# Performance work log

Measured on AMD Instinct MI355X. Metric: run time of the kernel, lower is better.

Reference implementation:

```python
import jax, jax.numpy as jnp
import numpy as np


def setup_inputs() -> dict:
    key = jax.random.key(0)
    k1, k2, k3, k4 = jax.random.split(key, 4)
    B, T, C, H = 8, 2048, 1024, 64
    x = jax.random.normal(k1, (B, T, C), dtype=jnp.float32)
    # nn.Linear weights, stored as (in, out) for x @ W
    Wk = jax.random.normal(k2, (C, H), dtype=jnp.float32) * (C ** -0.5)
    Wq = jax.random.normal(k3, (C, H), dtype=jnp.float32) * (C ** -0.5)
    Wv = jax.random.normal(k4, (C, H), dtype=jnp.float32) * (C ** -0.5)
    return {"x": x, "Wk": Wk, "Wq": Wq, "Wv": Wv}


def reference(x, Wk, Wq, Wv):
    B, T, C = x.shape
    k = x @ Wk  # [B,T,H]
    q = x @ Wq  # [B,T,H]
    v = x @ Wv  # [B,T,H]
    # NOTE: original scales by C**-0.5 (full embed dim), not head_size**-0.5
    wei = jnp.einsum("bth,bsh->bts", q, k) * (C ** -0.5)  # [B,T,T]
    causal = jnp.tril(jnp.ones((T, T), dtype=bool))
    wei = jnp.where(causal, wei, -jnp.inf)
    wei = jax.nn.softmax(wei, axis=-1)
    # dropout is identity in eval/reference mode
    out = jnp.einsum("bts,bsh->bth", wei, v)  # [B,T,H]
    return out
```

## Files before the change

### kernel.cpp

```cpp
#include <hip/hip_runtime.h>
#include <hip/hip_bf16.h>
#include <math.h>

#define B_ 8
#define T_ 2048
#define C_ 1024
#define H_ 64
#define M_ (B_*T_)

typedef __attribute__((ext_vector_type(8))) short short8;
typedef __attribute__((ext_vector_type(4))) float f32x4;
typedef unsigned int u32;

__device__ __forceinline__ unsigned short f2bf(float f) {
    u32 u = __builtin_bit_cast(u32, f);
    u += 0x7FFFu + ((u >> 16) & 1u);
    return (unsigned short)(u >> 16);
}

__device__ __forceinline__ void gl2lds16(const void* g, void* l) {
    __builtin_amdgcn_global_load_lds(
        (const __attribute__((address_space(1))) u32*)g,
        (__attribute__((address_space(3))) u32*)l, 16, 0, 0);
}

__global__ __launch_bounds__(256) void wconv(
    const float* __restrict__ Wk, const float* __restrict__ Wq,
    const float* __restrict__ Wv, unsigned short* __restrict__ wb)
{
    __shared__ unsigned short lt[64][64];
    const int mat = blockIdx.x >> 4;
    const int k0  = (blockIdx.x & 15) * 64;
    const float* src = (mat == 0) ? Wk : (mat == 1 ? Wq : Wv);
    const float sc = (mat == 1) ? 0.03125f : 1.0f;
    const int tid = threadIdx.x;

    for (int it = 0; it < 16; ++it) {
        int idx = it * 256 + tid;
        int r = idx >> 6, cn = idx & 63;
        lt[cn][r] = f2bf(src[(size_t)(k0 + r) * H_ + cn] * sc);
    }
    __syncthreads();
    for (int g = 0; g < 2; ++g) {
        int n  = g * 32 + (tid >> 3);
        int kp = tid & 7;
        int ng = mat * 64 + n;
        short8 v = *reinterpret_cast<const short8*>(&lt[n][kp * 8]);
        char* dst = (char*)wb + (size_t)ng * 2048 + (k0 >> 6) * 128
                  + ((kp * 16) ^ ((ng & 7) << 4));
        *reinterpret_cast<short8*>(dst) = v;
    }
}

__global__ __launch_bounds__(256, 2) void qkv_mm(
    const float* __restrict__ x, const unsigned short* __restrict__ wb,
    unsigned short* __restrict__ kb, unsigned short* __restrict__ qb,
    unsigned short* __restrict__ vT)
{
    __shared__ __align__(16) unsigned short Ws[2][96 * 64];

    const int tid  = threadIdx.x;
    const int wid  = tid >> 6;
    const int lane = tid & 63;
    const int lr   = lane & 15;
    const int lg   = lane >> 4;
    const int mt   = blockIdx.x >> 1;
    const int bn   = blockIdx.x & 1;
    const int m0   = mt * 64;
    const int n0   = bn * 96;

    const float* xrow = x + (size_t)(m0 + wid * 16 + lr) * C_ + lg * 8;

    f32x4 acc[6];
    for (int c = 0; c < 6; ++c) acc[c] = (f32x4){0.f, 0.f, 0.f, 0.f};

    float4 xa = *reinterpret_cast<const float4*>(xrow);
    float4 xb2 = *reinterpret_cast<const float4*>(xrow + 4);
    float4 xc = *reinterpret_cast<const float4*>(xrow + 32);
    float4 xd = *reinterpret_cast<const float4*>(xrow + 36);
    for (int p = 0; p < 3; ++p) {
        int c = p * 256 + tid;
        gl2lds16((const char*)wb + (size_t)(n0 + (c >> 3)) * 2048 + (c & 7) * 16,
                 (char*)&Ws[0][0] + c * 16);
    }

    for (int t = 0; t < 16; ++t) {
        __syncthreads();
        float4 na, nb, nc, nd;
        if (t < 15) {
            const float* xn = xrow + (t + 1) * 64;
            na = *reinterpret_cast<const float4*>(xn);
            nb = *reinterpret_cast<const float4*>(xn + 4);
            nc = *reinterpret_cast<const float4*>(xn + 32);
            nd = *reinterpret_cast<const float4*>(xn + 36);
            int buf = (t + 1) & 1;
            for (int p = 0; p < 3; ++p) {
                int c = p * 256 + tid;
                gl2lds16((const char*)wb + (size_t)(n0 + (c >> 3)) * 2048
                             + (size_t)(t + 1) * 128 + (c & 7) * 16,
                         (char*)&Ws[buf][0] + c * 16);
            }
        }

        short8 af0, af1;
        af0[0] = (short)f2bf(xa.x); af0[1] = (short)f2bf(xa.y);
        af0[2] = (short)f2bf(xa.z); af0[3] = (short)f2bf(xa.w);
        af0[4] = (short)f2bf(xb2.x); af0[5] = (short)f2bf(xb2.y);
        af0[6] = (short)f2bf(xb2.z); af0[7] = (short)f2bf(xb2.w);
        af1[0] = (short)f2bf(xc.x); af1[1] = (short)f2bf(xc.y);
        af1[2] = (short)f2bf(xc.z); af1[3] = (short)f2bf(xc.w);
        af1[4] = (short)f2bf(xd.x); af1[5] = (short)f2bf(xd.y);
        af1[6] = (short)f2bf(xd.z); af1[7] = (short)f2bf(xd.w);

        const char* wbuf = (const char*)&Ws[t & 1][0];
        #pragma unroll
        for (int kc = 0; kc < 2; ++kc) {
            short8 afc = kc ? af1 : af0;
            #pragma unroll
            for (int ct = 0; ct < 6; ++ct) {
                int n = ct * 16 + lr;
                short8 bf = *reinterpret_cast<const short8*>(
                    wbuf + n * 128 + ((kc * 64 + lg * 16) ^ ((n & 7) << 4)));
                acc[ct] = __builtin_amdgcn_mfma_f32_16x16x32_bf16(afc, bf, acc[ct], 0, 0, 0);
            }
        }
        xa = na; xb2 = nb; xc = nc; xd = nd;
    }

    for (int ct = 0; ct < 6; ++ct) {
        int ng = n0 + ct * 16 + lr;
        int col = ng & 63;
        for (int i = 0; i < 4; ++i) {
            int m = m0 + wid * 16 + lg * 4 + i;
            unsigned short val = f2bf(acc[ct][i]);
            if (ng < 64)       kb[(size_t)m * H_ + col] = val;
            else if (ng < 128) qb[(size_t)m * H_ + col] = val;
            else               vT[((size_t)(m >> 11) * H_ + col) * T_ + (m & (T_ - 1))] = val;
        }
    }
}

__global__ __launch_bounds__(256, 2) void attn4(
    const unsigned short* __restrict__ kb,
    const unsigned short* __restrict__ qb,
    const unsigned short* __restrict__ vT,
    float* __restrict__ out)
{
    __shared__ __align__(16) unsigned short Ps[4][16][72];
    __shared__ float Om[4][16][64];
    __shared__ float Mv[4][16], Lv[4][16], Fac[4][16], InvL[16];

    const int tid  = threadIdx.x;
    const int wid  = tid >> 6;
    const int lane = tid & 63;
    const int lr   = lane & 15;
    const int lg   = lane >> 4;
    const int b    = blockIdx.y;
    const int bx   = blockIdx.x;
    const int tile = (bx & 1) ? (127 - (bx >> 1)) : (bx >> 1);
    const int q0   = tile * 16;
    const int nsteps = (tile >> 2) + 1;
    const size_t base = (size_t)b * T_ * H_;
    const unsigned short* vTb = vT + (size_t)b * H_ * T_;

    short8 qf[2];
    #pragma unroll
    for (int kc = 0; kc < 2; ++kc)
        qf[kc] = *reinterpret_cast<const short8*>(
            qb + base + (size_t)(q0 + lr) * H_ + kc * 32 + lg * 8);

    f32x4 o[4];
    float mrun[4], lrun[4];
    for (int dt = 0; dt < 4; ++dt) o[dt] = (f32x4){0.f, 0.f, 0.f, 0.f};
    for (int i = 0; i < 4; ++i) { mrun[i] = -INFINITY; lrun[i] = 0.f; }

    for (int s = wid; s < nsteps; s += 4) {
        const int kv0 = s * 64;

        short8 kf[2][4];
        #pragma unroll
        for (int kc = 0; kc < 2; ++kc)
            #pragma unroll
            for (int kt = 0; kt < 4; ++kt)
                kf[kc][kt] = *reinterpret_cast<const short8*>(
                    kb + base + (size_t)(kv0 + kt * 16 + lr) * H_ + kc * 32 + lg * 8);

        f32x4 sv4[4];
        for (int kt = 0; kt < 4; ++kt) sv4[kt] = (f32x4){0.f, 0.f, 0.f, 0.f};
        #pragma unroll
        for (int kc = 0; kc < 2; ++kc)
            #pragma unroll
            for (int kt = 0; kt < 4; ++kt)
                sv4[kt] = __builtin_amdgcn_mfma_f32_16x16x32_bf16(qf[kc], kf[kc][kt], sv4[kt], 0, 0, 0);

        short8 vf[2][4];
        #pragma unroll
        for (int kc = 0; kc < 2; ++kc)
            #pragma unroll
            for (int dt = 0; dt < 4; ++dt)
                vf[kc][dt] = *reinterpret_cast<const short8*>(
                    vTb + (size_t)(dt * 16 + lr) * T_ + kv0 + kc * 32 + lg * 8);

        const bool need_mask = (s == nsteps - 1);

        for (int i = 0; i < 4; ++i) {
            int row = q0 + lg * 4 + i;
            float sv[4];
            float mx = -INFINITY;
            if (need_mask) {
                for (int kt = 0; kt < 4; ++kt) {
                    int key = kv0 + kt * 16 + lr;
                    float v = (key <= row) ? sv4[kt][i] : -INFINITY;
                    sv[kt] = v;
                    mx = fmaxf(mx, v);
                }
            } else {
                for (int kt = 0; kt < 4; ++kt) {
                    sv[kt] = sv4[kt][i];
                    mx = fmaxf(mx, sv[kt]);
                }
            }
            for (int d = 8; d; d >>= 1) mx = fmaxf(mx, __shfl_xor(mx, d));
            float mn  = fmaxf(mrun[i], mx);
            float fac = __expf(mrun[i] - mn);
            float rs  = 0.f;
            for (int kt = 0; kt < 4; ++kt) {
                float p = __expf(sv[kt] - mn);
                rs += p;
                Ps[wid][lg * 4 + i][kt * 16 + lr] = f2bf(p);
            }
            for (int d = 8; d; d >>= 1) rs += __shfl_xor(rs, d);
            lrun[i] = lrun[i] * fac + rs;
            mrun[i] = mn;
            for (int dt = 0; dt < 4; ++dt)
                o[dt][i] *= fac;
        }

        #pragma unroll
        for (int kc = 0; kc < 2; ++kc) {
            short8 pf = *reinterpret_cast<const short8*>(&Ps[wid][lr][kc * 32 + lg * 8]);
            #pragma unroll
            for (int dt = 0; dt < 4; ++dt)
                o[dt] = __builtin_amdgcn_mfma_f32_16x16x32_bf16(pf, vf[kc][dt], o[dt], 0, 0, 0);
        }
    }

    for (int dt = 0; dt < 4; ++dt)
        for (int i = 0; i < 4; ++i)
            Om[wid][lg * 4 + i][dt * 16 + lr] = o[dt][i];
    if (lr == 0)
        for (int i = 0; i < 4; ++i) {
            Mv[wid][lg * 4 + i] = mrun[i];
            Lv[wid][lg * 4 + i] = lrun[i];
        }
    __syncthreads();
    if (tid < 16) {
        float M = Mv[0][tid];
        for (int w = 1; w < 4; ++w) M = fmaxf(M, Mv[w][tid]);
        float L = 0.f;
        for (int w = 0; w < 4; ++w) {
            float f = __expf(Mv[w][tid] - M);
            Fac[w][tid] = f;
            L += Lv[w][tid] * f;
        }
        InvL[tid] = 1.0f / L;
    }
    __syncthreads();
    for (int e = 0; e < 4; ++e) {
        int idx = e * 256 + tid;
        int row = idx >> 6, d = idx & 63;
        float v = 0.f;
        for (int w = 0; w < 4; ++w) v += Om[w][row][d] * Fac[w][row];
        out[base + (size_t)(q0 + row) * H_ + d] = v * InvL[row];
    }
}

extern "C" void kernel_launch(void* const* d_in, const int* in_sizes, int n_in,
                              void* d_out, int out_size, void* d_ws, size_t ws_size,
                              hipStream_t stream) {
    const float* x  = (const float*)d_in[0];
    const float* Wk = (const float*)d_in[1];
    const float* Wq = (const float*)d_in[2];
    const float* Wv = (const float*)d_in[3];
    float* out = (float*)d_out;

    unsigned short* kb = (unsigned short*)d_ws;
    unsigned short* qb = kb + (size_t)M_ * H_;
    unsigned short* vT = qb + (size_t)M_ * H_;
    unsigned short* wb = vT + (size_t)M_ * H_;

    wconv<<<48, 256, 0, stream>>>(Wk, Wq, Wv, wb);
    qkv_mm<<<512, 256, 0, stream>>>(x, wb, kb, qb, vT);
    attn4<<<dim3(128, B_), 256, 0, stream>>>(kb, qb, vT, out);
}
```

Measured before the change: 179.5 us.

## Widen QKV GEMM tile, pipeline loads, split attention into single-wave blocks plus merge

```diff
diff --git a/kernel.cpp b/kernel.cpp
--- a/kernel.cpp
+++ b/kernel.cpp
@@ -16,6 +16,10 @@
     u32 u = __builtin_bit_cast(u32, f);
     u += 0x7FFFu + ((u >> 16) & 1u);
     return (unsigned short)(u >> 16);
+}
+__device__ __forceinline__ float bf2f(unsigned short h) {
+    u32 u = ((u32)h) << 16;
+    return __builtin_bit_cast(float, u);
 }
 
 __device__ __forceinline__ void gl2lds16(const void* g, void* l) {
@@ -52,114 +56,119 @@
     }
 }
 
-__global__ __launch_bounds__(256, 2) void qkv_mm(
+#define LOADX(R0,R1,R2,R3,t) {                                        \
+    const float* p_ = xrow + (t) * 64;                                \
+    R0 = *reinterpret_cast<const float4*>(p_);                        \
+    R1 = *reinterpret_cast<const float4*>(p_ + 4);                    \
+    R2 = *reinterpret_cast<const float4*>(p_ + 32);                   \
+    R3 = *reinterpret_cast<const float4*>(p_ + 36); }
+
+#define STAGEW(buf, t) {                                              \
+    _Pragma("unroll") for (int p_ = 0; p_ < 6; ++p_) {                \
+        int c_ = p_ * 256 + tid;                                      \
+        gl2lds16((const char*)wb + (size_t)(c_ >> 3) * 2048           \
+                     + (size_t)(t) * 128 + (c_ & 7) * 16,             \
+                 (char*)&Ws[buf][0] + c_ * 16);                       \
+    } }
+
+__global__ __launch_bounds__(256) void qkv_mm(
     const float* __restrict__ x, const unsigned short* __restrict__ wb,
     unsigned short* __restrict__ kb, unsigned short* __restrict__ qb,
     unsigned short* __restrict__ vT)
 {
-    __shared__ __align__(16) unsigned short Ws[2][96 * 64];
+    __shared__ __align__(16) unsigned short Ws[2][192 * 64];
 
     const int tid  = threadIdx.x;
     const int wid  = tid >> 6;
     const int lane = tid & 63;
     const int lr   = lane & 15;
     const int lg   = lane >> 4;
-    const int mt   = blockIdx.x >> 1;
-    const int bn   = blockIdx.x & 1;
-    const int m0   = mt * 64;
-    const int n0   = bn * 96;
+    const int m0   = blockIdx.x * 64;
 
     const float* xrow = x + (size_t)(m0 + wid * 16 + lr) * C_ + lg * 8;
 
-    f32x4 acc[6];
-    for (int c = 0; c < 6; ++c) acc[c] = (f32x4){0.f, 0.f, 0.f, 0.f};
-
-    float4 xa = *reinterpret_cast<const float4*>(xrow);
-    float4 xb2 = *reinterpret_cast<const float4*>(xrow + 4);
-    float4 xc = *reinterpret_cast<const float4*>(xrow + 32);
-    float4 xd = *reinterpret_cast<const float4*>(xrow + 36);
-    for (int p = 0; p < 3; ++p) {
-        int c = p * 256 + tid;
-        gl2lds16((const char*)wb + (size_t)(n0 + (c >> 3)) * 2048 + (c & 7) * 16,
-                 (char*)&Ws[0][0] + c * 16);
-    }
-
+    f32x4 acc[12];
+    #pragma unroll
+    for (int c = 0; c < 12; ++c) acc[c] = (f32x4){0.f, 0.f, 0.f, 0.f};
+
+    float4 xA0, xA1, xA2, xA3, xB0, xB1, xB2, xB3, xC0, xC1, xC2, xC3;
+
+    LOADX(xA0, xA1, xA2, xA3, 0);
+    __builtin_amdgcn_sched_barrier(0);
+    STAGEW(0, 0);
+    __builtin_amdgcn_sched_barrier(0);
+    LOADX(xB0, xB1, xB2, xB3, 1);
+    __builtin_amdgcn_sched_barrier(0);
+
+    #pragma unroll
     for (int t = 0; t < 16; ++t) {
-        __syncthreads();
-        float4 na, nb, nc, nd;
-        if (t < 15) {
-            const float* xn = xrow + (t + 1) * 64;
-            na = *reinterpret_cast<const float4*>(xn);
-            nb = *reinterpret_cast<const float4*>(xn + 4);
-            nc = *reinterpret_cast<const float4*>(xn + 32);
-            nd = *reinterpret_cast<const float4*>(xn + 36);
-            int buf = (t + 1) & 1;
-            for (int p = 0; p < 3; ++p) {
-                int c = p * 256 + tid;
-                gl2lds16((const char*)wb + (size_t)(n0 + (c >> 3)) * 2048
-                             + (size_t)(t + 1) * 128 + (c & 7) * 16,
-                         (char*)&Ws[buf][0] + c * 16);
-            }
-        }
+        if (t < 15) asm volatile("s_waitcnt vmcnt(4) lgkmcnt(0)" ::: "memory");
+        else        asm volatile("s_waitcnt vmcnt(0) lgkmcnt(0)" ::: "memory");
+        __builtin_amdgcn_s_barrier();
+        __builtin_amdgcn_sched_barrier(0);
+        if (t < 15) { STAGEW((t + 1) & 1, t + 1); }
+        __builtin_amdgcn_sched_barrier(0);
+        if (t < 14) { LOADX(xC0, xC1, xC2, xC3, t + 2); }
+        __builtin_amdgcn_sched_barrier(0);
 
         short8 af0, af1;
-        af0[0] = (short)f2bf(xa.x); af0[1] = (short)f2bf(xa.y);
-        af0[2] = (short)f2bf(xa.z); af0[3] = (short)f2bf(xa.w);
-        af0[4] = (short)f2bf(xb2.x); af0[5] = (short)f2bf(xb2.y);
-        af0[6] = (short)f2bf(xb2.z); af0[7] = (short)f2bf(xb2.w);
-        af1[0] = (short)f2bf(xc.x); af1[1] = (short)f2bf(xc.y);
-        af1[2] = (short)f2bf(xc.z); af1[3] = (short)f2bf(xc.w);
-        af1[4] = (short)f2bf(xd.x); af1[5] = (short)f2bf(xd.y);
-        af1[6] = (short)f2bf(xd.z); af1[7] = (short)f2bf(xd.w);
+        af0[0] = (short)f2bf(xA0.x); af0[1] = (short)f2bf(xA0.y);
+        af0[2] = (short)f2bf(xA0.z); af0[3] = (short)f2bf(xA0.w);
+        af0[4] = (short)f2bf(xA1.x); af0[5] = (short)f2bf(xA1.y);
+        af0[6] = (short)f2bf(xA1.z); af0[7] = (short)f2bf(xA1.w);
+        af1[0] = (short)f2bf(xA2.x); af1[1] = (short)f2bf(xA2.y);
+        af1[2] = (short)f2bf(xA2.z); af1[3] = (short)f2bf(xA2.w);
+        af1[4] = (short)f2bf(xA3.x); af1[5] = (short)f2bf(xA3.y);
+        af1[6] = (short)f2bf(xA3.z); af1[7] = (short)f2bf(xA3.w);
 
         const char* wbuf = (const char*)&Ws[t & 1][0];
         #pragma unroll
         for (int kc = 0; kc < 2; ++kc) {
             short8 afc = kc ? af1 : af0;
             #pragma unroll
-            for (int ct = 0; ct < 6; ++ct) {
+            for (int ct = 0; ct < 12; ++ct) {
                 int n = ct * 16 + lr;
                 short8 bf = *reinterpret_cast<const short8*>(
                     wbuf + n * 128 + ((kc * 64 + lg * 16) ^ ((n & 7) << 4)));
                 acc[ct] = __builtin_amdgcn_mfma_f32_16x16x32_bf16(afc, bf, acc[ct], 0, 0, 0);
             }
         }
-        xa = na; xb2 = nb; xc = nc; xd = nd;
-    }
-
-    for (int ct = 0; ct < 6; ++ct) {
-        int ng = n0 + ct * 16 + lr;
-        int col = ng & 63;
+        xA0 = xB0; xA1 = xB1; xA2 = xB2; xA3 = xB3;
+        xB0 = xC0; xB1 = xC1; xB2 = xC2; xB3 = xC3;
+    }
+
+    #pragma unroll
+    for (int ct = 0; ct < 12; ++ct) {
+        int n = ct * 16 + lr;
+        int col = n & 63;
+        #pragma unroll
         for (int i = 0; i < 4; ++i) {
             int m = m0 + wid * 16 + lg * 4 + i;
             unsigned short val = f2bf(acc[ct][i]);
-            if (ng < 64)       kb[(size_t)m * H_ + col] = val;
-            else if (ng < 128) qb[(size_t)m * H_ + col] = val;
-            else               vT[((size_t)(m >> 11) * H_ + col) * T_ + (m & (T_ - 1))] = val;
-        }
-    }
-}
-
-__global__ __launch_bounds__(256, 2) void attn4(
+            if (n < 64)       kb[(size_t)m * H_ + col] = val;
+            else if (n < 128) qb[(size_t)m * H_ + col] = val;
+            else              vT[((size_t)(m >> 11) * H_ + col) * T_ + (m & (T_ - 1))] = val;
+        }
+    }
+}
+
+__global__ __launch_bounds__(64) void attn7(
     const unsigned short* __restrict__ kb,
     const unsigned short* __restrict__ qb,
     const unsigned short* __restrict__ vT,
-    float* __restrict__ out)
+    unsigned short* __restrict__ opart,
+    float* __restrict__ ml)
 {
-    __shared__ __align__(16) unsigned short Ps[4][16][72];
-    __shared__ float Om[4][16][64];
-    __shared__ float Mv[4][16], Lv[4][16], Fac[4][16], InvL[16];
-
-    const int tid  = threadIdx.x;
-    const int wid  = tid >> 6;
-    const int lane = tid & 63;
+    __shared__ __align__(16) unsigned short Ps[16][72];
+
+    const int lane = threadIdx.x;
     const int lr   = lane & 15;
     const int lg   = lane >> 4;
-    const int b    = blockIdx.y;
-    const int bx   = blockIdx.x;
-    const int tile = (bx & 1) ? (127 - (bx >> 1)) : (bx >> 1);
+    const int s0   = blockIdx.x;
+    const int tile = 127 - blockIdx.y;
+    const int b    = blockIdx.z;
     const int q0   = tile * 16;
-    const int nsteps = (tile >> 2) + 1;
+    const int nst  = (tile >> 2) + 1;
     const size_t base = (size_t)b * T_ * H_;
     const unsigned short* vTb = vT + (size_t)b * H_ * T_;
 
@@ -174,40 +183,30 @@
     for (int dt = 0; dt < 4; ++dt) o[dt] = (f32x4){0.f, 0.f, 0.f, 0.f};
     for (int i = 0; i < 4; ++i) { mrun[i] = -INFINITY; lrun[i] = 0.f; }
 
-    for (int s = wid; s < nsteps; s += 4) {
+    for (int s = s0; s < nst; s += 4) {
         const int kv0 = s * 64;
 
-        short8 kf[2][4];
-        #pragma unroll
-        for (int kc = 0; kc < 2; ++kc)
-            #pragma unroll
-            for (int kt = 0; kt < 4; ++kt)
-                kf[kc][kt] = *reinterpret_cast<const short8*>(
+        f32x4 sv4[4];
+        #pragma unroll
+        for (int kt = 0; kt < 4; ++kt) sv4[kt] = (f32x4){0.f, 0.f, 0.f, 0.f};
+        #pragma unroll
+        for (int kc = 0; kc < 2; ++kc) {
+            #pragma unroll
+            for (int kt = 0; kt < 4; ++kt) {
+                short8 kf = *reinterpret_cast<const short8*>(
                     kb + base + (size_t)(kv0 + kt * 16 + lr) * H_ + kc * 32 + lg * 8);
-
-        f32x4 sv4[4];
-        for (int kt = 0; kt < 4; ++kt) sv4[kt] = (f32x4){0.f, 0.f, 0.f, 0.f};
-        #pragma unroll
-        for (int kc = 0; kc < 2; ++kc)
-            #pragma unroll
-            for (int kt = 0; kt < 4; ++kt)
-                sv4[kt] = __builtin_amdgcn_mfma_f32_16x16x32_bf16(qf[kc], kf[kc][kt], sv4[kt], 0, 0, 0);
-
-        short8 vf[2][4];
-        #pragma unroll
-        for (int kc = 0; kc < 2; ++kc)
-            #pragma unroll
-            for (int dt = 0; dt < 4; ++dt)
-                vf[kc][dt] = *reinterpret_cast<const short8*>(
-                    vTb + (size_t)(dt * 16 + lr) * T_ + kv0 + kc * 32 + lg * 8);
-
-        const bool need_mask = (s == nsteps - 1);
-
+                sv4[kt] = __builtin_amdgcn_mfma_f32_16x16x32_bf16(qf[kc], kf, sv4[kt], 0, 0, 0);
+            }
+        }
+
+        const bool need_mask = (s == nst - 1);
+        #pragma unroll
         for (int i = 0; i < 4; ++i) {
             int row = q0 + lg * 4 + i;
             float sv[4];
             float mx = -INFINITY;
             if (need_mask) {
+                #pragma unroll
                 for (int kt = 0; kt < 4; ++kt) {
                     int key = kv0 + kt * 16 + lr;
                     float v = (key <= row) ? sv4[kt][i] : -INFINITY;
@@ -215,6 +214,7 @@
                     mx = fmaxf(mx, v);
                 }
             } else {
+                #pragma unroll
                 for (int kt = 0; kt < 4; ++kt) {
                     sv[kt] = sv4[kt][i];
                     mx = fmaxf(mx, sv[kt]);
@@ -224,55 +224,73 @@
             float mn  = fmaxf(mrun[i], mx);
             float fac = __expf(mrun[i] - mn);
             float rs  = 0.f;
+            #pragma unroll
             for (int kt = 0; kt < 4; ++kt) {
                 float p = __expf(sv[kt] - mn);
                 rs += p;
-                Ps[wid][lg * 4 + i][kt * 16 + lr] = f2bf(p);
+                Ps[lg * 4 + i][kt * 16 + lr] = f2bf(p);
             }
             for (int d = 8; d; d >>= 1) rs += __shfl_xor(rs, d);
             lrun[i] = lrun[i] * fac + rs;
             mrun[i] = mn;
+            #pragma unroll
             for (int dt = 0; dt < 4; ++dt)
                 o[dt][i] *= fac;
         }
 
         #pragma unroll
         for (int kc = 0; kc < 2; ++kc) {
-            short8 pf = *reinterpret_cast<const short8*>(&Ps[wid][lr][kc * 32 + lg * 8]);
-            #pragma unroll
-            for (int dt = 0; dt < 4; ++dt)
-                o[dt] = __builtin_amdgcn_mfma_f32_16x16x32_bf16(pf, vf[kc][dt], o[dt], 0, 0, 0);
-        }
-    }
-
-    for (int dt = 0; dt < 4; ++dt)
-        for (int i = 0; i < 4; ++i)
-            Om[wid][lg * 4 + i][dt * 16 + lr] = o[dt][i];
-    if (lr == 0)
+            short8 pf = *reinterpret_cast<const short8*>(&Ps[lr][kc * 32 + lg * 8]);
+            #pragma unroll
+            for (int dt = 0; dt < 4; ++dt) {
+                short8 vf = *reinterpret_cast<const short8*>(
+                    vTb + (size_t)(dt * 16 + lr) * T_ + kv0 + kc * 32 + lg * 8);
+                o[dt] = __builtin_amdgcn_mfma_f32_16x16x32_bf16(pf, vf, o[dt], 0, 0, 0);
+            }
+        }
+    }
+
+    unsigned short* op = opart + ((size_t)s0 * M_ + (size_t)b * T_ + q0) * H_;
+    #pragma unroll
+    for (int i = 0; i < 4; ++i)
+        #pragma unroll
+        for (int dt = 0; dt < 4; ++dt)
+            op[(size_t)(lg * 4 + i) * H_ + dt * 16 + lr] = f2bf(o[dt][i]);
+    if (lr == 0) {
+        float* mlp = ml + ((size_t)s0 * M_ + (size_t)b * T_ + q0) * 2;
+        #pragma unroll
         for (int i = 0; i < 4; ++i) {
-            Mv[wid][lg * 4 + i] = mrun[i];
-            Lv[wid][lg * 4 + i] = lrun[i];
-        }
-    __syncthreads();
-    if (tid < 16) {
-        float M = Mv[0][tid];
-        for (int w = 1; w < 4; ++w) M = fmaxf(M, Mv[w][tid]);
-        float L = 0.f;
-        for (int w = 0; w < 4; ++w) {
-            float f = __expf(Mv[w][tid] - M);
-            Fac[w][tid] = f;
-            L += Lv[w][tid] * f;
-        }
-        InvL[tid] = 1.0f / L;
-    }
-    __syncthreads();
-    for (int e = 0; e < 4; ++e) {
-        int idx = e * 256 + tid;
-        int row = idx >> 6, d = idx & 63;
-        float v = 0.f;
-        for (int w = 0; w < 4; ++w) v += Om[w][row][d] * Fac[w][row];
-        out[base + (size_t)(q0 + row) * H_ + d] = v * InvL[row];
-    }
+            mlp[(lg * 4 + i) * 2 + 0] = mrun[i];
+            mlp[(lg * 4 + i) * 2 + 1] = lrun[i];
+        }
+    }
+}
+
+__global__ __launch_bounds__(256) void attn_merge(
+    const unsigned short* __restrict__ opart,
+    const float* __restrict__ ml,
+    float* __restrict__ out)
+{
+    const int idx = blockIdx.x * 256 + threadIdx.x;
+    const int row = idx >> 6;
+    const int col = idx & 63;
+
+    float mv[4], lv[4];
+    float M = -INFINITY;
+    #pragma unroll
+    for (int s = 0; s < 4; ++s) {
+        mv[s] = ml[((size_t)s * M_ + row) * 2 + 0];
+        lv[s] = ml[((size_t)s * M_ + row) * 2 + 1];
+        M = fmaxf(M, mv[s]);
+    }
+    float L = 0.f, acc = 0.f;
+    #pragma unroll
+    for (int s = 0; s < 4; ++s) {
+        float fac = __expf(mv[s] - M);
+        L += lv[s] * fac;
+        acc += bf2f(opart[(size_t)s * M_ * H_ + (size_t)row * H_ + col]) * fac;
+    }
+    out[idx] = acc / L;
 }
 
 extern "C" void kernel_launch(void* const* d_in, const int* in_sizes, int n_in,
@@ -284,12 +302,15 @@
     const float* Wv = (const float*)d_in[3];
     float* out = (float*)d_out;
 
-    unsigned short* kb = (unsigned short*)d_ws;
-    unsigned short* qb = kb + (size_t)M_ * H_;
-    unsigned short* vT = qb + (size_t)M_ * H_;
-    unsigned short* wb = vT + (size_t)M_ * H_;
+    unsigned short* kb    = (unsigned short*)d_ws;
+    unsigned short* qb    = kb + (size_t)M_ * H_;
+    unsigned short* vT    = qb + (size_t)M_ * H_;
+    unsigned short* wb    = vT + (size_t)M_ * H_;
+    unsigned short* opart = wb + (size_t)192 * C_;
+    float*          ml    = (float*)(opart + (size_t)4 * M_ * H_);
 
     wconv<<<48, 256, 0, stream>>>(Wk, Wq, Wv, wb);
-    qkv_mm<<<512, 256, 0, stream>>>(x, wb, kb, qb, vT);
-    attn4<<<dim3(128, B_), 256, 0, stream>>>(kb, qb, vT, out);
-}
+    qkv_mm<<<256, 256, 0, stream>>>(x, wb, kb, qb, vT);
+    attn7<<<dim3(4, 128, B_), 64, 0, stream>>>(kb, qb, vT, opart, ml);
+    attn_merge<<<M_ * H_ / 256, 256, 0, stream>>>(opart, ml, out);
+}
```

After: 162.8 us. 9.3% less time.
